# Kernel optimization log

Measured on AMD Instinct MI355X. Metric: run time of the kernel, lower is better.

Reference implementation:

```python
import jax, jax.numpy as jnp
import numpy as np

D_MODEL = 1024
NHEAD = 16
HEAD_DIM = D_MODEL // NHEAD
D_FF = 4 * D_MODEL
B, L = 2, 2048
EPS = 1e-5


def layer_norm(x, g, b):
    mu = jnp.mean(x, axis=-1, keepdims=True)
    var = jnp.mean(jnp.square(x - mu), axis=-1, keepdims=True)
    return (x - mu) * jax.lax.rsqrt(var + EPS) * g + b


def setup_inputs() -> dict:
    key = jax.random.key(0)
    ks = jax.random.split(key, 12)
    s = 1.0 / np.sqrt(D_MODEL)
    inp = {
        "x": jax.random.normal(ks[0], (B, L, D_MODEL), jnp.float32),
        "mask": jnp.tril(jnp.ones((L, L), jnp.int32)),  # causal mask; 0 => masked
        "Wq": jax.random.normal(ks[1], (D_MODEL, D_MODEL), jnp.float32) * s,
        "bq": jnp.zeros((D_MODEL,), jnp.float32),
        "Wk": jax.random.normal(ks[2], (D_MODEL, D_MODEL), jnp.float32) * s,
        "bk": jnp.zeros((D_MODEL,), jnp.float32),
        "Wv": jax.random.normal(ks[3], (D_MODEL, D_MODEL), jnp.float32) * s,
        "bv": jnp.zeros((D_MODEL,), jnp.float32),
        "Wo": jax.random.normal(ks[4], (D_MODEL, D_MODEL), jnp.float32) * s,
        "bo": jnp.zeros((D_MODEL,), jnp.float32),
        "g1": jnp.ones((D_MODEL,), jnp.float32),
        "b1": jnp.zeros((D_MODEL,), jnp.float32),
        "g2": jnp.ones((D_MODEL,), jnp.float32),
        "b2": jnp.zeros((D_MODEL,), jnp.float32),
        "W1": jax.random.normal(ks[5], (D_MODEL, D_FF), jnp.float32) * s,
        "bf1": jnp.zeros((D_FF,), jnp.float32),
        "W2": jax.random.normal(ks[6], (D_FF, D_MODEL), jnp.float32) * (1.0 / np.sqrt(D_FF)),
        "bf2": jnp.zeros((D_MODEL,), jnp.float32),
    }
    return inp


def reference(x, mask, Wq, bq, Wk, bk, Wv, bv, Wo, bo, g1, b1, g2, b2, W1, bf1, W2, bf2):
    # Pre-norm attention (dropout = identity in eval mode)
    nx = layer_norm(x, g1, b1)
    Bb, Ll, Dd = nx.shape
    def heads(t):
        return t.reshape(Bb, Ll, NHEAD, HEAD_DIM).transpose(0, 2, 1, 3)  # [B,H,L,hd]
    q = heads(nx @ Wq + bq)
    k = heads(nx @ Wk + bk)
    v = heads(nx @ Wv + bv)
    scale = 1.0 / np.sqrt(HEAD_DIM)
    attn = jnp.einsum("bhqd,bhkd->bhqk", q, k) * scale  # [B,H,L,L]
    attn = jnp.where(mask[:Ll, :Ll] == 0, jnp.float32(-1e9), attn)
    attn = jax.nn.softmax(attn, axis=-1)
    attn_out = jnp.einsum("bhqk,bhkd->bhqd", attn, v)
    attn_out = attn_out.transpose(0, 2, 1, 3).reshape(Bb, Ll, Dd)
    x = x + (attn_out @ Wo + bo)
    # Pre-norm FFN with exact GELU (torch nn.GELU default)
    nx2 = layer_norm(x, g2, b2)
    h = jax.nn.gelu(nx2 @ W1 + bf1, approximate=False)
    x = x + (h @ W2 + bf2)
    return x
```

## Files before the change

### kernel.cpp

```cpp
#include <hip/hip_runtime.h>
#include <hip/hip_bf16.h>

__device__ __forceinline__ float bfbits2f(unsigned short u) {
  return __uint_as_float(((unsigned int)u) << 16);
}
__device__ __forceinline__ unsigned short f2bfbits(float f) {
  unsigned int x = __float_as_uint(f);
  unsigned int r = (x + 0x7FFFu + ((x >> 16) & 1u)) >> 16;
  return (unsigned short)r;
}

typedef short bf16x8 __attribute__((ext_vector_type(8)));
typedef float f32x4 __attribute__((ext_vector_type(4)));

__device__ __forceinline__ void gload_lds16(const unsigned short* g, unsigned short* l) {
  __builtin_amdgcn_global_load_lds((const __attribute__((address_space(1))) unsigned int*)g,
                                   (__attribute__((address_space(3))) unsigned int*)l, 16, 0, 0);
}

__global__ __launch_bounds__(256) void transpose_cast_k(const float* __restrict__ in,
                                                        unsigned short* __restrict__ out,
                                                        int K, int N) {
  __shared__ float tile[32][33];
  int n0 = blockIdx.x * 32, k0 = blockIdx.y * 32;
  int tx = threadIdx.x, ty = threadIdx.y;
#pragma unroll
  for (int j = 0; j < 32; j += 8)
    tile[ty + j][tx] = in[(size_t)(k0 + ty + j) * N + n0 + tx];
  __syncthreads();
#pragma unroll
  for (int j = 0; j < 32; j += 8)
    out[(size_t)(n0 + ty + j) * K + k0 + tx] = f2bfbits(tile[tx][ty + j]);
}

__global__ void concat_bias_k(const float* __restrict__ bq, const float* __restrict__ bk,
                              const float* __restrict__ bv, float* __restrict__ out) {
  int i = blockIdx.x * 256 + threadIdx.x;
  if (i < 1024) {
    out[i] = bq[i];
    out[1024 + i] = bk[i];
    out[2048 + i] = bv[i];
  }
}

__global__ __launch_bounds__(256) void ln_k(const float* __restrict__ x,
                                            const float* __restrict__ g,
                                            const float* __restrict__ bb,
                                            unsigned short* __restrict__ out) {
  __shared__ float red[8];
  int row = blockIdx.x, tid = threadIdx.x;
  int lane = tid & 63, wv = tid >> 6;
  float4 v = reinterpret_cast<const float4*>(x + (size_t)row * 1024)[tid];
  float s = v.x + v.y + v.z + v.w;
#pragma unroll
  for (int off = 32; off >= 1; off >>= 1) s += __shfl_xor(s, off, 64);
  if (lane == 0) red[wv] = s;
  __syncthreads();
  float mu = (red[0] + red[1] + red[2] + red[3]) * (1.0f / 1024.0f);
  float a0 = v.x - mu, a1 = v.y - mu, a2 = v.z - mu, a3 = v.w - mu;
  float sq = a0 * a0 + a1 * a1 + a2 * a2 + a3 * a3;
#pragma unroll
  for (int off = 32; off >= 1; off >>= 1) sq += __shfl_xor(sq, off, 64);
  if (lane == 0) red[4 + wv] = sq;
  __syncthreads();
  float var = (red[4] + red[5] + red[6] + red[7]) * (1.0f / 1024.0f);
  float rstd = rsqrtf(var + 1e-5f);
  float4 gv = reinterpret_cast<const float4*>(g)[tid];
  float4 bv = reinterpret_cast<const float4*>(bb)[tid];
  ushort4 u;
  u.x = f2bfbits(a0 * rstd * gv.x + bv.x);
  u.y = f2bfbits(a1 * rstd * gv.y + bv.y);
  u.z = f2bfbits(a2 * rstd * gv.z + bv.z);
  u.w = f2bfbits(a3 * rstd * gv.w + bv.w);
  *reinterpret_cast<ushort4*>(out + (size_t)row * 1024 + tid * 4) = u;
}

template <int MODE>
__global__ __launch_bounds__(256) void gemm_bt_k(const unsigned short* __restrict__ A,
                                                 const unsigned short* __restrict__ BT,
                                                 const float* __restrict__ bias,
                                                 const float* __restrict__ resid,
                                                 void* __restrict__ Cout,
                                                 int M, int N, int K) {
  __shared__ unsigned short As[128 * 64];
  __shared__ unsigned short Bs[128 * 64];
  int tid = threadIdx.x;
  int wid = tid >> 6, lane = tid & 63;
  int m0 = blockIdx.x * 128, n0 = blockIdx.y * 128;
  int wr = wid >> 1, wc = wid & 1;
  int cl = lane & 15, g = lane >> 4;

  f32x4 acc[4][4];
#pragma unroll
  for (int i = 0; i < 4; i++)
#pragma unroll
    for (int j = 0; j < 4; j++) acc[i][j] = {0.f, 0.f, 0.f, 0.f};

  for (int k0 = 0; k0 < K; k0 += 64) {
#pragma unroll
    for (int i = 0; i < 4; ++i) {
      int c = i * 256 + tid;
      int r = c >> 3;
      int cc = (c & 7) * 8;
      gload_lds16(&A[(size_t)(m0 + r) * K + k0 + cc], &As[(i * 256 + wid * 64) * 8]);
      gload_lds16(&BT[(size_t)(n0 + r) * K + k0 + cc], &Bs[(i * 256 + wid * 64) * 8]);
    }
    __syncthreads();
#pragma unroll
    for (int kk = 0; kk < 64; kk += 32) {
      bf16x8 af[4], bfr[4];
#pragma unroll
      for (int mt = 0; mt < 4; mt++)
        af[mt] = *reinterpret_cast<const bf16x8*>(&As[(wr * 64 + mt * 16 + cl) * 64 + kk + g * 8]);
#pragma unroll
      for (int nt = 0; nt < 4; nt++)
        bfr[nt] = *reinterpret_cast<const bf16x8*>(&Bs[(wc * 64 + nt * 16 + cl) * 64 + kk + g * 8]);
#pragma unroll
      for (int mt = 0; mt < 4; mt++)
#pragma unroll
        for (int nt = 0; nt < 4; nt++)
          acc[mt][nt] = __builtin_amdgcn_mfma_f32_16x16x32_bf16(af[mt], bfr[nt], acc[mt][nt], 0, 0, 0);
    }
    __syncthreads();
  }

#pragma unroll
  for (int mt = 0; mt < 4; mt++) {
#pragma unroll
    for (int nt = 0; nt < 4; nt++) {
#pragma unroll
      for (int r = 0; r < 4; r++) {
        int gr = m0 + wr * 64 + mt * 16 + g * 4 + r;
        int gc = n0 + wc * 64 + nt * 16 + cl;
        float v = acc[mt][nt][r] + bias[gc];
        if constexpr (MODE == 1) {
          v += resid[(size_t)gr * N + gc];
          ((float*)Cout)[(size_t)gr * N + gc] = v;
        } else if constexpr (MODE == 2) {
          v = 0.5f * v * (1.0f + erff(v * 0.70710678118654752f));
          ((unsigned short*)Cout)[(size_t)gr * N + gc] = f2bfbits(v);
        } else {
          ((unsigned short*)Cout)[(size_t)gr * N + gc] = f2bfbits(v);
        }
      }
    }
  }
}

__global__ __launch_bounds__(256) void attn_k(const unsigned short* __restrict__ qkv,
                                              unsigned short* __restrict__ out) {
  __shared__ unsigned short Ks[64 * 64];
  __shared__ unsigned short Vt[64 * 64];
  __shared__ unsigned short Ps[4][16 * 64];

  const int L = 2048, RS = 3072;
  int tid = threadIdx.x;
  int wid = tid >> 6, lane = tid & 63;
  int qt = (int)gridDim.x - 1 - (int)blockIdx.x;
  int h = blockIdx.y, b = blockIdx.z;
  int q0 = qt * 64;
  int qw = q0 + wid * 16;
  int g = lane >> 4;
  int cl = lane & 15;

  const unsigned short* qbase = qkv + (size_t)(b * L + qw + cl) * RS + h * 64 + g * 8;
  bf16x8 qf0 = *reinterpret_cast<const bf16x8*>(qbase);
  bf16x8 qf1 = *reinterpret_cast<const bf16x8*>(qbase + 32);

  float m_r[4], l_r[4];
  f32x4 o_acc[4];
#pragma unroll
  for (int r = 0; r < 4; ++r) { m_r[r] = -1e30f; l_r[r] = 0.f; }
#pragma unroll
  for (int d = 0; d < 4; ++d) o_acc[d] = {0.f, 0.f, 0.f, 0.f};

  const unsigned short* kvbase = qkv + (size_t)(b * L) * RS + 1024 + h * 64;
  int ntiles = qt + 1;

  for (int tt = 0; tt < ntiles; ++tt) {
    int kb = tt * 64;
#pragma unroll
    for (int it = 0; it < 2; ++it) {
      int idx = it * 256 + tid;
      int r = idx >> 3, ch = idx & 7;
      gload_lds16(kvbase + (size_t)(kb + r) * RS + (ch ^ (r & 7)) * 8,
                  &Ks[(it * 256 + wid * 64) * 8]);
    }
    {
      int kcol = tid & 63;
      int d0 = wid * 16;
      const unsigned short* vsrc = kvbase + (size_t)(kb + kcol) * RS + 1024 + d0;
      bf16x8 v0 = *reinterpret_cast<const bf16x8*>(vsrc);
      bf16x8 v1 = *reinterpret_cast<const bf16x8*>(vsrc + 8);
#pragma unroll
      for (int j = 0; j < 8; ++j) {
        int d = d0 + j;
        Vt[d * 64 + 8 * ((kcol >> 3) ^ (d & 7)) + (kcol & 7)] = (unsigned short)v0[j];
        int d2 = d0 + 8 + j;
        Vt[d2 * 64 + 8 * ((kcol >> 3) ^ (d2 & 7)) + (kcol & 7)] = (unsigned short)v1[j];
      }
    }
    __syncthreads();

    f32x4 sacc[4];
#pragma unroll
    for (int kblk = 0; kblk < 4; ++kblk) sacc[kblk] = {0.f, 0.f, 0.f, 0.f};
#pragma unroll
    for (int kblk = 0; kblk < 4; ++kblk) {
      int kcol = kblk * 16 + cl;
      bf16x8 kf0 = *reinterpret_cast<const bf16x8*>(&Ks[kcol * 64 + 8 * (g ^ (kcol & 7))]);
      bf16x8 kf1 = *reinterpret_cast<const bf16x8*>(&Ks[kcol * 64 + 8 * ((g + 4) ^ (kcol & 7))]);
      sacc[kblk] = __builtin_amdgcn_mfma_f32_16x16x32_bf16(qf0, kf0, sacc[kblk], 0, 0, 0);
      sacc[kblk] = __builtin_amdgcn_mfma_f32_16x16x32_bf16(qf1, kf1, sacc[kblk], 0, 0, 0);
    }

    bool lastTile = (tt == ntiles - 1);
    float rowmax[4];
#pragma unroll
    for (int r = 0; r < 4; ++r) {
      float mx = -1e30f;
#pragma unroll
      for (int kblk = 0; kblk < 4; ++kblk) {
        float s = sacc[kblk][r] * 0.125f;
        if (lastTile && (kblk * 16 + cl > wid * 16 + g * 4 + r)) s = -1e30f;
        sacc[kblk][r] = s;
        mx = fmaxf(mx, s);
      }
      rowmax[r] = mx;
    }
#pragma unroll
    for (int off = 1; off <= 8; off <<= 1)
#pragma unroll
      for (int r = 0; r < 4; ++r) rowmax[r] = fmaxf(rowmax[r], __shfl_xor(rowmax[r], off, 64));
#pragma unroll
    for (int r = 0; r < 4; ++r) {
      float mnew = fmaxf(m_r[r], rowmax[r]);
      float corr = __expf(m_r[r] - mnew);
      m_r[r] = mnew;
      int q_l = g * 4 + r;
      float rs = 0.f;
#pragma unroll
      for (int kblk = 0; kblk < 4; ++kblk) {
        float p = __expf(sacc[kblk][r] - mnew);
        rs += p;
        int k_l = kblk * 16 + cl;
        Ps[wid][q_l * 64 + 8 * ((k_l >> 3) ^ (q_l & 7)) + (k_l & 7)] = f2bfbits(p);
      }
#pragma unroll
      for (int off = 1; off <= 8; off <<= 1) rs += __shfl_xor(rs, off, 64);
      l_r[r] = l_r[r] * corr + rs;
#pragma unroll
      for (int dblk = 0; dblk < 4; ++dblk) o_acc[dblk][r] *= corr;
    }
    asm volatile("s_waitcnt lgkmcnt(0)" ::: "memory");
    __builtin_amdgcn_sched_barrier(0);

    bf16x8 pa0 = *reinterpret_cast<const bf16x8*>(&Ps[wid][cl * 64 + 8 * (g ^ (cl & 7))]);
    bf16x8 pa1 = *reinterpret_cast<const bf16x8*>(&Ps[wid][cl * 64 + 8 * ((g + 4) ^ (cl & 7))]);
#pragma unroll
    for (int dblk = 0; dblk < 4; ++dblk) {
      int d = dblk * 16 + cl;
      bf16x8 vb0 = *reinterpret_cast<const bf16x8*>(&Vt[d * 64 + 8 * (g ^ (d & 7))]);
      bf16x8 vb1 = *reinterpret_cast<const bf16x8*>(&Vt[d * 64 + 8 * ((g + 4) ^ (d & 7))]);
      o_acc[dblk] = __builtin_amdgcn_mfma_f32_16x16x32_bf16(pa0, vb0, o_acc[dblk], 0, 0, 0);
      o_acc[dblk] = __builtin_amdgcn_mfma_f32_16x16x32_bf16(pa1, vb1, o_acc[dblk], 0, 0, 0);
    }
    __syncthreads();
  }

#pragma unroll
  for (int r = 0; r < 4; ++r) {
    float linv = 1.0f / l_r[r];
    int orow = qw + g * 4 + r;
    unsigned short* obase = out + (size_t)(b * L + orow) * 1024 + h * 64;
#pragma unroll
    for (int dblk = 0; dblk < 4; ++dblk)
      obase[dblk * 16 + cl] = f2bfbits(o_acc[dblk][r] * linv);
  }
}

extern "C" void kernel_launch(void* const* d_in, const int* in_sizes, int n_in,
                              void* d_out, int out_size, void* d_ws, size_t ws_size,
                              hipStream_t stream) {
  const float* x = (const float*)d_in[0];
  const float* Wq = (const float*)d_in[2];
  const float* bq = (const float*)d_in[3];
  const float* Wk = (const float*)d_in[4];
  const float* bk = (const float*)d_in[5];
  const float* Wv = (const float*)d_in[6];
  const float* bv = (const float*)d_in[7];
  const float* Wo = (const float*)d_in[8];
  const float* bo = (const float*)d_in[9];
  const float* g1 = (const float*)d_in[10];
  const float* b1 = (const float*)d_in[11];
  const float* g2 = (const float*)d_in[12];
  const float* b2 = (const float*)d_in[13];
  const float* W1 = (const float*)d_in[14];
  const float* bf1 = (const float*)d_in[15];
  const float* W2 = (const float*)d_in[16];
  const float* bf2 = (const float*)d_in[17];
  float* out = (float*)d_out;

  const int M = 4096;
  char* ws = (char*)d_ws;
  size_t off = 0;
  auto alloc = [&](size_t bytes) -> void* {
    void* p = ws + off;
    off += (bytes + 255) & ~(size_t)255;
    return p;
  };
  unsigned short* WqkvT = (unsigned short*)alloc((size_t)3072 * 1024 * 2);
  unsigned short* WoT = (unsigned short*)alloc((size_t)1024 * 1024 * 2);
  unsigned short* W1T = (unsigned short*)alloc((size_t)4096 * 1024 * 2);
  unsigned short* W2T = (unsigned short*)alloc((size_t)1024 * 4096 * 2);
  float* bqkv = (float*)alloc(3072 * 4);
  unsigned short* actA = (unsigned short*)alloc((size_t)M * 1024 * 2);
  unsigned short* actB = (unsigned short*)alloc((size_t)M * 4096 * 2);

  dim3 tb(32, 8);
  transpose_cast_k<<<dim3(32, 32), tb, 0, stream>>>(Wq, WqkvT, 1024, 1024);
  transpose_cast_k<<<dim3(32, 32), tb, 0, stream>>>(Wk, WqkvT + (size_t)1024 * 1024, 1024, 1024);
  transpose_cast_k<<<dim3(32, 32), tb, 0, stream>>>(Wv, WqkvT + (size_t)2048 * 1024, 1024, 1024);
  transpose_cast_k<<<dim3(32, 32), tb, 0, stream>>>(Wo, WoT, 1024, 1024);
  transpose_cast_k<<<dim3(128, 32), tb, 0, stream>>>(W1, W1T, 1024, 4096);
  transpose_cast_k<<<dim3(32, 128), tb, 0, stream>>>(W2, W2T, 4096, 1024);
  concat_bias_k<<<dim3(4), dim3(256), 0, stream>>>(bq, bk, bv, bqkv);

  ln_k<<<dim3(M), dim3(256), 0, stream>>>(x, g1, b1, actA);
  gemm_bt_k<0><<<dim3(M / 128, 3072 / 128), dim3(256), 0, stream>>>(actA, WqkvT, bqkv, nullptr, actB, M, 3072, 1024);
  attn_k<<<dim3(32, 16, 2), dim3(256), 0, stream>>>(actB, actA);
  gemm_bt_k<1><<<dim3(M / 128, 1024 / 128), dim3(256), 0, stream>>>(actA, WoT, bo, x, out, M, 1024, 1024);
  ln_k<<<dim3(M), dim3(256), 0, stream>>>(out, g2, b2, actA);
  gemm_bt_k<2><<<dim3(M / 128, 4096 / 128), dim3(256), 0, stream>>>(actA, W1T, bf1, nullptr, actB, M, 4096, 1024);
  gemm_bt_k<1><<<dim3(M / 128, 1024 / 128), dim3(256), 0, stream>>>(actB, W2T, bf2, out, out, M, 1024, 4096);
}
```

Before: 533.2 us.

## Double-buffer K tiles and use 128-query blocks in causal attention

The attention kernel now runs 8 waves per block over 128 query rows and keeps two K buffers in LDS. The next K tile is prefetched with global_load_lds, and the next V tile is held in registers while the current tile is computed. Fully unmasked tiles skip the per-element mask test, and the scale is folded into a log2e factor so exp2f can be used. The four 1024x1024 weight transposes are merged into one launch. The aim is to hide global load latency and cut per-tile overhead. The cost is more LDS, coarser causal work imbalance (the grid halves), and an extra barrier per tile.

```diff
diff --git a/kernel.cpp b/kernel.cpp
--- a/kernel.cpp
+++ b/kernel.cpp
@@ -31,6 +31,27 @@
 #pragma unroll
   for (int j = 0; j < 32; j += 8)
     out[(size_t)(n0 + ty + j) * K + k0 + tx] = f2bfbits(tile[tx][ty + j]);
+}
+
+__global__ __launch_bounds__(256) void transpose_cast4_k(const float* __restrict__ w0,
+                                                         const float* __restrict__ w1,
+                                                         const float* __restrict__ w2,
+                                                         const float* __restrict__ w3,
+                                                         unsigned short* __restrict__ o012,
+                                                         unsigned short* __restrict__ o3) {
+  __shared__ float tile[32][33];
+  int z = blockIdx.z;
+  const float* in = (z == 0) ? w0 : (z == 1) ? w1 : (z == 2) ? w2 : w3;
+  unsigned short* out = (z < 3) ? (o012 + (size_t)z * 1024 * 1024) : o3;
+  int n0 = blockIdx.x * 32, k0 = blockIdx.y * 32;
+  int tx = threadIdx.x, ty = threadIdx.y;
+#pragma unroll
+  for (int j = 0; j < 32; j += 8)
+    tile[ty + j][tx] = in[(size_t)(k0 + ty + j) * 1024 + n0 + tx];
+  __syncthreads();
+#pragma unroll
+  for (int j = 0; j < 32; j += 8)
+    out[(size_t)(n0 + ty + j) * 1024 + k0 + tx] = f2bfbits(tile[tx][ty + j]);
 }
 
 __global__ void concat_bias_k(const float* __restrict__ bq, const float* __restrict__ bk,
@@ -147,26 +168,40 @@
   }
 }
 
-__global__ __launch_bounds__(256) void attn_k(const unsigned short* __restrict__ qkv,
+__global__ __launch_bounds__(512) void attn_k(const unsigned short* __restrict__ qkv,
                                               unsigned short* __restrict__ out) {
-  __shared__ unsigned short Ks[64 * 64];
+  __shared__ unsigned short Ks[2][64 * 64];
   __shared__ unsigned short Vt[64 * 64];
-  __shared__ unsigned short Ps[4][16 * 64];
+  __shared__ unsigned short Ps[8][16 * 64];
 
   const int L = 2048, RS = 3072;
+  const float SCALE = 0.125f * 1.44269504f;
   int tid = threadIdx.x;
   int wid = tid >> 6, lane = tid & 63;
   int qt = (int)gridDim.x - 1 - (int)blockIdx.x;
   int h = blockIdx.y, b = blockIdx.z;
-  int q0 = qt * 64;
+  int q0 = qt * 128;
   int qw = q0 + wid * 16;
   int g = lane >> 4;
   int cl = lane & 15;
 
+  const unsigned short* kbase = qkv + (size_t)(b * L) * RS + 1024 + h * 64;
+  const unsigned short* vbase = kbase + 1024;
+
   const unsigned short* qbase = qkv + (size_t)(b * L + qw + cl) * RS + h * 64 + g * 8;
   bf16x8 qf0 = *reinterpret_cast<const bf16x8*>(qbase);
   bf16x8 qf1 = *reinterpret_cast<const bf16x8*>(qbase + 32);
 
+  int kr = tid >> 3, kch = tid & 7;
+  size_t ksrc_off = (size_t)kr * RS + ((kch ^ (kr & 7)) * 8);
+  int vk = tid & 63, vd0 = (tid >> 6) * 8;
+  int vaddr[8];
+#pragma unroll
+  for (int j = 0; j < 8; ++j) {
+    int d = vd0 + j;
+    vaddr[j] = d * 64 + 8 * ((vk >> 3) ^ (d & 7)) + (vk & 7);
+  }
+
   float m_r[4], l_r[4];
   f32x4 o_acc[4];
 #pragma unroll
@@ -174,33 +209,26 @@
 #pragma unroll
   for (int d = 0; d < 4; ++d) o_acc[d] = {0.f, 0.f, 0.f, 0.f};
 
-  const unsigned short* kvbase = qkv + (size_t)(b * L) * RS + 1024 + h * 64;
-  int ntiles = qt + 1;
-
-  for (int tt = 0; tt < ntiles; ++tt) {
+  int nt = 2 * qt + 2;
+
+  gload_lds16(kbase + ksrc_off, &Ks[0][wid * 512]);
+  bf16x8 vreg = *reinterpret_cast<const bf16x8*>(vbase + (size_t)vk * RS + vd0);
+
+  int buf = 0;
+  for (int tt = 0; tt < nt; ++tt) {
     int kb = tt * 64;
-#pragma unroll
-    for (int it = 0; it < 2; ++it) {
-      int idx = it * 256 + tid;
-      int r = idx >> 3, ch = idx & 7;
-      gload_lds16(kvbase + (size_t)(kb + r) * RS + (ch ^ (r & 7)) * 8,
-                  &Ks[(it * 256 + wid * 64) * 8]);
-    }
-    {
-      int kcol = tid & 63;
-      int d0 = wid * 16;
-      const unsigned short* vsrc = kvbase + (size_t)(kb + kcol) * RS + 1024 + d0;
-      bf16x8 v0 = *reinterpret_cast<const bf16x8*>(vsrc);
-      bf16x8 v1 = *reinterpret_cast<const bf16x8*>(vsrc + 8);
-#pragma unroll
-      for (int j = 0; j < 8; ++j) {
-        int d = d0 + j;
-        Vt[d * 64 + 8 * ((kcol >> 3) ^ (d & 7)) + (kcol & 7)] = (unsigned short)v0[j];
-        int d2 = d0 + 8 + j;
-        Vt[d2 * 64 + 8 * ((kcol >> 3) ^ (d2 & 7)) + (kcol & 7)] = (unsigned short)v1[j];
-      }
-    }
-    __syncthreads();
+    asm volatile("s_waitcnt vmcnt(0)" ::: "memory");
+    __builtin_amdgcn_s_barrier();
+    __builtin_amdgcn_sched_barrier(0);
+
+#pragma unroll
+    for (int j = 0; j < 8; ++j) Vt[vaddr[j]] = (unsigned short)vreg[j];
+
+    if (tt + 1 < nt) {
+      int kb1 = (size_t)(tt + 1) * 64;
+      gload_lds16(kbase + (size_t)kb1 * RS + ksrc_off, &Ks[buf ^ 1][wid * 512]);
+      vreg = *reinterpret_cast<const bf16x8*>(vbase + (size_t)(kb1 + vk) * RS + vd0);
+    }
 
     f32x4 sacc[4];
 #pragma unroll
@@ -208,25 +236,39 @@
 #pragma unroll
     for (int kblk = 0; kblk < 4; ++kblk) {
       int kcol = kblk * 16 + cl;
-      bf16x8 kf0 = *reinterpret_cast<const bf16x8*>(&Ks[kcol * 64 + 8 * (g ^ (kcol & 7))]);
-      bf16x8 kf1 = *reinterpret_cast<const bf16x8*>(&Ks[kcol * 64 + 8 * ((g + 4) ^ (kcol & 7))]);
+      bf16x8 kf0 = *reinterpret_cast<const bf16x8*>(&Ks[buf][kcol * 64 + 8 * (g ^ (kcol & 7))]);
+      bf16x8 kf1 = *reinterpret_cast<const bf16x8*>(&Ks[buf][kcol * 64 + 8 * ((g + 4) ^ (kcol & 7))]);
       sacc[kblk] = __builtin_amdgcn_mfma_f32_16x16x32_bf16(qf0, kf0, sacc[kblk], 0, 0, 0);
       sacc[kblk] = __builtin_amdgcn_mfma_f32_16x16x32_bf16(qf1, kf1, sacc[kblk], 0, 0, 0);
     }
 
-    bool lastTile = (tt == ntiles - 1);
     float rowmax[4];
-#pragma unroll
-    for (int r = 0; r < 4; ++r) {
-      float mx = -1e30f;
-#pragma unroll
-      for (int kblk = 0; kblk < 4; ++kblk) {
-        float s = sacc[kblk][r] * 0.125f;
-        if (lastTile && (kblk * 16 + cl > wid * 16 + g * 4 + r)) s = -1e30f;
-        sacc[kblk][r] = s;
-        mx = fmaxf(mx, s);
+    if (kb + 63 <= qw) {
+#pragma unroll
+      for (int r = 0; r < 4; ++r) {
+        float mx = -1e30f;
+#pragma unroll
+        for (int kblk = 0; kblk < 4; ++kblk) {
+          float s = sacc[kblk][r] * SCALE;
+          sacc[kblk][r] = s;
+          mx = fmaxf(mx, s);
+        }
+        rowmax[r] = mx;
       }
-      rowmax[r] = mx;
+    } else {
+#pragma unroll
+      for (int r = 0; r < 4; ++r) {
+        float mx = -1e30f;
+        int qg = qw + g * 4 + r;
+#pragma unroll
+        for (int kblk = 0; kblk < 4; ++kblk) {
+          float s = sacc[kblk][r] * SCALE;
+          if (kb + kblk * 16 + cl > qg) s = -1e30f;
+          sacc[kblk][r] = s;
+          mx = fmaxf(mx, s);
+        }
+        rowmax[r] = mx;
+      }
     }
 #pragma unroll
     for (int off = 1; off <= 8; off <<= 1)
@@ -235,13 +277,13 @@
 #pragma unroll
     for (int r = 0; r < 4; ++r) {
       float mnew = fmaxf(m_r[r], rowmax[r]);
-      float corr = __expf(m_r[r] - mnew);
+      float corr = exp2f(m_r[r] - mnew);
       m_r[r] = mnew;
       int q_l = g * 4 + r;
       float rs = 0.f;
 #pragma unroll
       for (int kblk = 0; kblk < 4; ++kblk) {
-        float p = __expf(sacc[kblk][r] - mnew);
+        float p = exp2f(sacc[kblk][r] - mnew);
         rs += p;
         int k_l = kblk * 16 + cl;
         Ps[wid][q_l * 64 + 8 * ((k_l >> 3) ^ (q_l & 7)) + (k_l & 7)] = f2bfbits(p);
@@ -252,7 +294,9 @@
 #pragma unroll
       for (int dblk = 0; dblk < 4; ++dblk) o_acc[dblk][r] *= corr;
     }
+
     asm volatile("s_waitcnt lgkmcnt(0)" ::: "memory");
+    __builtin_amdgcn_s_barrier();
     __builtin_amdgcn_sched_barrier(0);
 
     bf16x8 pa0 = *reinterpret_cast<const bf16x8*>(&Ps[wid][cl * 64 + 8 * (g ^ (cl & 7))]);
@@ -265,7 +309,7 @@
       o_acc[dblk] = __builtin_amdgcn_mfma_f32_16x16x32_bf16(pa0, vb0, o_acc[dblk], 0, 0, 0);
       o_acc[dblk] = __builtin_amdgcn_mfma_f32_16x16x32_bf16(pa1, vb1, o_acc[dblk], 0, 0, 0);
     }
-    __syncthreads();
+    buf ^= 1;
   }
 
 #pragma unroll
@@ -318,17 +362,14 @@
   unsigned short* actB = (unsigned short*)alloc((size_t)M * 4096 * 2);
 
   dim3 tb(32, 8);
-  transpose_cast_k<<<dim3(32, 32), tb, 0, stream>>>(Wq, WqkvT, 1024, 1024);
-  transpose_cast_k<<<dim3(32, 32), tb, 0, stream>>>(Wk, WqkvT + (size_t)1024 * 1024, 1024, 1024);
-  transpose_cast_k<<<dim3(32, 32), tb, 0, stream>>>(Wv, WqkvT + (size_t)2048 * 1024, 1024, 1024);
-  transpose_cast_k<<<dim3(32, 32), tb, 0, stream>>>(Wo, WoT, 1024, 1024);
+  transpose_cast4_k<<<dim3(32, 32, 4), tb, 0, stream>>>(Wq, Wk, Wv, Wo, WqkvT, WoT);
   transpose_cast_k<<<dim3(128, 32), tb, 0, stream>>>(W1, W1T, 1024, 4096);
   transpose_cast_k<<<dim3(32, 128), tb, 0, stream>>>(W2, W2T, 4096, 1024);
   concat_bias_k<<<dim3(4), dim3(256), 0, stream>>>(bq, bk, bv, bqkv);
 
   ln_k<<<dim3(M), dim3(256), 0, stream>>>(x, g1, b1, actA);
   gemm_bt_k<0><<<dim3(M / 128, 3072 / 128), dim3(256), 0, stream>>>(actA, WqkvT, bqkv, nullptr, actB, M, 3072, 1024);
-  attn_k<<<dim3(32, 16, 2), dim3(256), 0, stream>>>(actB, actA);
+  attn_k<<<dim3(16, 16, 2), dim3(512), 0, stream>>>(actB, actA);
   gemm_bt_k<1><<<dim3(M / 128, 1024 / 128), dim3(256), 0, stream>>>(actA, WoT, bo, x, out, M, 1024, 1024);
   ln_k<<<dim3(M), dim3(256), 0, stream>>>(out, g2, b2, actA);
   gemm_bt_k<2><<<dim3(M / 128, 4096 / 128), dim3(256), 0, stream>>>(actA, W1T, bf1, nullptr, actB, M, 4096, 1024);
```

Measured after the change: 531.5 us. No clear change (-0.3%).
